# Optimization experiments

Measured on AMD Instinct MI355X. Metric: run time of the kernel, lower is better.

Reference implementation:

```python
import jax, jax.numpy as jnp
import numpy as np

N0, N1, N2, N3 = 8192, 32768, 65536, 65536
CUM = (N0, N0 + N1, N0 + N1 + N2, N0 + N1 + N2 + N3)  # nodes through hop k
NTOT = CUM[3]
EH = (131072, 262144, 262144)                          # edges per hop (per edge type)
ECUM = (EH[0], EH[0] + EH[1], EH[0] + EH[1] + EH[2])
ETOT = ECUM[2]
C, H, T = 64, 256, 3
HH = H // 2
B, L = 16, 512  # N0 == B * L: equal-length note sequences per graph
LN_EPS = 1e-5


def _ln(x, w, b):
    m = x.mean(-1, keepdims=True)
    v = x.var(-1, keepdims=True)
    return (x - m) / jnp.sqrt(v + LN_EPS) * w + b


def _seg_mean(msgs, dst, n):
    s = jax.ops.segment_sum(msgs, dst, num_segments=n)
    cnt = jax.ops.segment_sum(jnp.ones(dst.shape, msgs.dtype), dst, num_segments=n)
    return s / jnp.maximum(cnt, 1.0)[:, None]


def _l2(x):
    return x / jnp.maximum(jnp.linalg.norm(x, axis=-1, keepdims=True), 1e-12)


def _gru_dir(x, wih, whh, bih, bhh, reverse):
    # x: [B, Lt, Din]; torch gate order (r, z, n)
    gi = jnp.einsum('bld,gd->blg', x, wih) + bih
    gi = jnp.moveaxis(gi, 1, 0)  # [Lt, B, 3*HH]
    h0 = jnp.zeros((x.shape[0], HH), x.dtype)

    def step(h, g):
        gh = h @ whh.T + bhh
        ir, iz, in_ = jnp.split(g, 3, -1)
        hr, hz, hn = jnp.split(gh, 3, -1)
        r = jax.nn.sigmoid(ir + hr)
        z = jax.nn.sigmoid(iz + hz)
        n = jnp.tanh(in_ + r * hn)
        hnew = (1.0 - z) * n + z * h
        return hnew, hnew

    _, ys = jax.lax.scan(step, h0, gi, reverse=reverse)
    return jnp.moveaxis(ys, 0, 1)  # [B, Lt, HH]


def _bigru(x, wih, whh, bih, bhh):
    f = _gru_dir(x, wih[0], whh[0], bih[0], bhh[0], False)
    bwd = _gru_dir(x, wih[1], whh[1], bih[1], bhh[1], True)
    return jnp.concatenate([f, bwd], -1)


def _forward(x, edge_index, batch_size, sage0_proj_w, sage0_proj_b, sage0_lw, sage0_lb,
             sage0_rw, sage_lw, sage_lb, sage_rw, ln_w, ln_b,
             gru_wih0, gru_whh0, gru_bih0, gru_bhh0,
             gru_wih1, gru_whh1, gru_bih1, gru_bhh1,
             rnn_norm_w, rnn_norm_b, mlp1_w, mlp1_b, mlp_ln_w, mlp_ln_b,
             mlp2_w, mlp2_b, cat_w, cat_b):
    # ---- hybrid GRU branch on seed notes (equal lengths -> pad == reshape) ----
    xs = x[:batch_size].reshape(B, L, C)
    h = _bigru(xs, gru_wih0, gru_whh0, gru_bih0, gru_bhh0)
    h = _bigru(h, gru_wih1, gru_whh1, gru_bih1, gru_bhh1)  # inter-layer dropout: eval mode
    h = _ln(h, rnn_norm_w, rnn_norm_b)
    h = _ln(jax.nn.relu(h @ mlp1_w + mlp1_b), mlp_ln_w, mlp_ln_b) @ mlp2_w + mlp2_b
    x_rnn = h.reshape(batch_size, H)

    # ---- GNN layer 0: SAGEConv(project=True, normalize=True), hetero mean over T types ----
    feat = x
    outs = []
    for t in range(T):
        src, dst = edge_index[t, 0], edge_index[t, 1]
        xp = jax.nn.relu(feat @ sage0_proj_w[t] + sage0_proj_b[t])
        agg = _seg_mean(xp[src], dst, NTOT)
        outs.append(_l2(agg @ sage0_lw[t] + sage0_lb[t] + feat @ sage0_rw[t]))
    feat = sum(outs) / T
    feat = _ln(jax.nn.relu(feat), ln_w[0], ln_b[0])  # dropout: eval mode (identity)

    # ---- layers 1..2 with trim_to_layer: drop last sampled hop each layer ----
    n_layer = (CUM[2], CUM[1])
    e_layer = (ECUM[1], ECUM[0])
    for i in range(2):
        n, e = n_layer[i], e_layer[i]
        feat = feat[:n]
        outs = []
        for t in range(T):
            src, dst = edge_index[t, 0, :e], edge_index[t, 1, :e]
            agg = _seg_mean(feat[src], dst, n)
            outs.append(agg @ sage_lw[i, t] + sage_lb[i, t] + feat @ sage_rw[i, t])
        feat = sum(outs) / T
        if i == 0:
            feat = _ln(jax.nn.relu(feat), ln_w[1], ln_b[1])
    x_gnn = feat[:batch_size]
    return jnp.concatenate([x_rnn, x_gnn], -1) @ cat_w + cat_b


def setup_inputs():
    key = jax.random.key(0)
    ks = iter(jax.random.split(key, 64))

    def nrm(shape, fan_in):
        return jax.random.normal(next(ks), shape, jnp.float32) / float(np.sqrt(fan_in))

    # hop-structured edges: hop k has src < CUM[k+1], dst < CUM[k]
    ei = []
    for t in range(T):
        rows, cols = [], []
        for k in range(3):
            rows.append(jax.random.randint(next(ks), (EH[k],), 0, CUM[k + 1]))
            cols.append(jax.random.randint(next(ks), (EH[k],), 0, CUM[k]))
        ei.append(jnp.stack([jnp.concatenate(rows), jnp.concatenate(cols)]))
    edge_index = jnp.stack(ei).astype(jnp.int32)

    return dict(
        x=jax.random.normal(next(ks), (NTOT, C), jnp.float32),
        edge_index=edge_index,
        batch=(jnp.arange(N0) // L).astype(jnp.int32),
        batch_size=N0,
        sage0_proj_w=nrm((T, C, C), C), sage0_proj_b=jnp.zeros((T, C), jnp.float32),
        sage0_lw=nrm((T, C, H), C), sage0_lb=jnp.zeros((T, H), jnp.float32),
        sage0_rw=nrm((T, C, H), C),
        sage_lw=nrm((2, T, H, H), H), sage_lb=jnp.zeros((2, T, H), jnp.float32),
        sage_rw=nrm((2, T, H, H), H),
        ln_w=jnp.ones((2, H), jnp.float32), ln_b=jnp.zeros((2, H), jnp.float32),
        gru_wih0=nrm((2, 3 * HH, C), C), gru_whh0=nrm((2, 3 * HH, HH), HH),
        gru_bih0=jnp.zeros((2, 3 * HH), jnp.float32), gru_bhh0=jnp.zeros((2, 3 * HH), jnp.float32),
        gru_wih1=nrm((2, 3 * HH, H), H), gru_whh1=nrm((2, 3 * HH, HH), HH),
        gru_bih1=jnp.zeros((2, 3 * HH), jnp.float32), gru_bhh1=jnp.zeros((2, 3 * HH), jnp.float32),
        rnn_norm_w=jnp.ones((H,), jnp.float32), rnn_norm_b=jnp.zeros((H,), jnp.float32),
        mlp1_w=nrm((H, H), H), mlp1_b=jnp.zeros((H,), jnp.float32),
        mlp_ln_w=jnp.ones((H,), jnp.float32), mlp_ln_b=jnp.zeros((H,), jnp.float32),
        mlp2_w=nrm((H, H), H), mlp2_b=jnp.zeros((H,), jnp.float32),
        cat_w=nrm((2 * H, H), 2 * H), cat_b=jnp.zeros((H,), jnp.float32),
    )


def reference(x, edge_index, batch, batch_size, sage0_proj_w, sage0_proj_b, sage0_lw,
              sage0_lb, sage0_rw, sage_lw, sage_lb, sage_rw, ln_w, ln_b,
              gru_wih0, gru_whh0, gru_bih0, gru_bhh0, gru_wih1, gru_whh1, gru_bih1,
              gru_bhh1, rnn_norm_w, rnn_norm_b, mlp1_w, mlp1_b, mlp_ln_w, mlp_ln_b,
              mlp2_w, mlp2_b, cat_w, cat_b):
    # batch encodes 16 equal-length (512) sequences; bincount/pad == reshape above
    return _forward(x, edge_index, batch_size, sage0_proj_w, sage0_proj_b, sage0_lw,
                    sage0_lb, sage0_rw, sage_lw, sage_lb, sage_rw, ln_w, ln_b,
                    gru_wih0, gru_whh0, gru_bih0, gru_bhh0, gru_wih1, gru_whh1,
                    gru_bih1, gru_bhh1, rnn_norm_w, rnn_norm_b, mlp1_w, mlp1_b,
                    mlp_ln_w, mlp_ln_b, mlp2_w, mlp2_b, cat_w, cat_b)
```

## Files before the change

kernel.cpp:

```cpp
#include <hip/hip_runtime.h>
#include <stdint.h>

typedef unsigned short u16;
typedef __attribute__((ext_vector_type(8))) short short8;
typedef __attribute__((ext_vector_type(4))) short short4v;
typedef __attribute__((ext_vector_type(4))) float float4v;

#define DEV static __device__ __forceinline__

DEV float bf2f(u16 u){ union { unsigned int i; float f; } c; c.i = ((unsigned int)u) << 16; return c.f; }
DEV u16 f2bf(float f){ union { float ff; unsigned int i; } c; c.ff = f;
  unsigned int x = c.i; return (u16)((x + 0x7fffu + ((x >> 16) & 1u)) >> 16); }

#define MFMA16(a,b,c) __builtin_amdgcn_mfma_f32_16x16x32_bf16((a),(b),(c),0,0,0)

#define ETOTC  655360
#define TSTRIDE 155648
#define NBINS   466944

struct SM {
  u16 As[64*72];
  u16 Bs[256*72];
  float redS[4][64];
  float redQ[4][64];
  float rowA[64], rowB[64];
};

__global__ void detect_dtype(const u16* __restrict__ xs, int* __restrict__ flag){
  __shared__ int sh[256];
  int t = threadIdx.x; int cnt = 0;
  for (int i = t; i < 4096; i += 256){
    u16 u = xs[i]; int e = (u >> 7) & 0xff;
    cnt += (u == 0 || (e >= 112 && e <= 143)) ? 1 : 0;
  }
  sh[t] = cnt; __syncthreads();
  for (int d = 128; d; d >>= 1){ if (t < d) sh[t] += sh[t+d]; __syncthreads(); }
  if (t == 0) flag[0] = (sh[0] >= 3686) ? 1 : 0;
}

DEV u16 scrub(u16 v){ int e = (v >> 7) & 0xff; return (e == 0xff) ? (u16)0 : v; }

struct WSrc { const void* p[28]; };
__device__ const int g_wcum[29] = {0,12288,12480,61632,62400,111552,504768,506304,899520,
  900032,900544,949696,1048000,1048768,1049536,1246144,1344448,1345216,1345984,1346240,
  1346496,1412032,1412288,1412544,1412800,1478336,1478592,1609664,1609920};

__global__ void convert_all(const void* __restrict__ xin, WSrc d,
                            const int* __restrict__ flag, u16* __restrict__ xout,
                            u16* __restrict__ wout){
  int b = blockIdx.x;
  if (b < 10752){
    int i = b*256 + threadIdx.x;
    u16 v[4];
    if (flag[0] == 1){
      short4v s = ((const short4v*)xin)[i];
#pragma unroll
      for (int j=0;j<4;j++) v[j] = scrub((u16)s[j]);
    } else {
      float4v f = ((const float4v*)xin)[i];
#pragma unroll
      for (int j=0;j<4;j++) v[j] = scrub(f2bf(f[j]));
    }
    short4v o; o[0]=(short)v[0]; o[1]=(short)v[1]; o[2]=(short)v[2]; o[3]=(short)v[3];
    ((short4v*)xout)[i] = o;
  } else {
    int i = (b - 10752)*256 + threadIdx.x;
    if (i >= 1609920) return;
    int lo = 0, hi = 28;
    while (hi - lo > 1){ int m = (lo+hi) >> 1; if (i >= g_wcum[m]) lo = m; else hi = m; }
    int off = i - g_wcum[lo];
    u16 v = (flag[0] == 1) ? ((const u16*)d.p[lo])[off]
                           : f2bf(((const float*)d.p[lo])[off]);
    wout[i] = scrub(v);
  }
}

__global__ void packT(const u16* __restrict__ in, u16* __restrict__ out, int K, int N){
  int i = blockIdx.x*256 + threadIdx.x;
  if (i < K*N){ int n = i / K, k = i - n*K; out[i] = in[(size_t)k*N + n]; }
}

__global__ void pack_lr(const u16* __restrict__ lw, const u16* __restrict__ rw,
                        u16* __restrict__ out, int F){
  int K2 = 2*F; long total = 3L*256*K2;
  long i = (long)blockIdx.x*256 + threadIdx.x;
  if (i < total){
    int k = (int)(i % K2); int n = (int)((i / K2) & 255); int t = (int)(i / ((long)K2*256));
    out[i] = (k < F) ? lw[((size_t)t*F + k)*256 + n]
                     : rw[((size_t)t*F + (k-F))*256 + n];
  }
}

DEV void hist_body(int gb, const int* __restrict__ ei, int* __restrict__ cnt){
  int g = gb*256 + threadIdx.x;
  int t = g / ETOTC, e = g - t*ETOTC;
  int dst = ei[(size_t)t*2*ETOTC + ETOTC + e];
  int base = t*TSTRIDE;
  atomicAdd(&cnt[base + dst], 1);
  if (e < 393216) atomicAdd(&cnt[base + 106496 + dst], 1);
  if (e < 131072) atomicAdd(&cnt[base + 147456 + dst], 1);
}

DEV void perm_body(int gb, const int* __restrict__ ei, const int* __restrict__ off,
                   int* __restrict__ slot, int* __restrict__ srcs){
  int g = gb*256 + threadIdx.x;
  int t = g / ETOTC, e = g - t*ETOTC;
  int dst = ei[(size_t)t*2*ETOTC + ETOTC + e];
  int src = ei[(size_t)t*2*ETOTC + e];
  int base = t*TSTRIDE;
  { int b = base + dst; srcs[off[b] + atomicAdd(&slot[b], 1)] = src; }
  if (e < 393216){ int b = base + 106496 + dst;
    srcs[off[b] + atomicAdd(&slot[b], 1)] = src; }
  if (e < 131072){ int b = base + 147456 + dst;
    srcs[off[b] + atomicAdd(&slot[b], 1)] = src; }
}

__global__ void scan_blocks(const int* __restrict__ cnt, int* __restrict__ off,
                            int* __restrict__ bsum, int n){
  __shared__ int sh[256];
  int t = threadIdx.x;
  int base = blockIdx.x*2048 + t*8;
  int v[8]; int tot = 0;
#pragma unroll
  for (int j=0;j<8;j++){ v[j] = (base+j < n) ? cnt[base+j] : 0; tot += v[j]; }
  sh[t] = tot; __syncthreads();
  for (int d=1; d<256; d<<=1){
    int y = (t>=d) ? sh[t-d] : 0; __syncthreads();
    sh[t] += y; __syncthreads();
  }
  int run = sh[t] - tot;
#pragma unroll
  for (int j=0;j<8;j++){ if (base+j < n) off[base+j] = run; run += v[j]; }
  if (t == 255) bsum[blockIdx.x] = sh[255];
}

__global__ void scan_top(int* __restrict__ bsum, int G){
  __shared__ int sh[256];
  int t = threadIdx.x;
  int v = (t < G) ? bsum[t] : 0;
  sh[t] = v; __syncthreads();
  for (int d=1; d<256; d<<=1){
    int y = (t>=d) ? sh[t-d] : 0; __syncthreads();
    sh[t] += y; __syncthreads();
  }
  if (t < G) bsum[t] = sh[t] - v;
}

__global__ void scan_add(int* __restrict__ off, const int* __restrict__ bsum, int n){
  int add = bsum[blockIdx.x];
  int base = blockIdx.x*2048 + threadIdx.x*8;
#pragma unroll
  for (int j=0;j<8;j++) if (base+j < n) off[base+j] += add;
}

template<int F>
DEV void gather_body(int w, int lane,
    const int* __restrict__ off, const int* __restrict__ cnt, const int* __restrict__ srcs,
    const u16* __restrict__ feat, int ld, u16* __restrict__ out)
{
  int st = off[w], c = cnt[w];
  float sc = 1.f / (float)(c < 1 ? 1 : c);
  if (F == 64) {
    float a = 0.f, b = 0.f;
    int i = 0;
    for (; i + 4 <= c; i += 4){
      int s0 = srcs[st+i], s1 = srcs[st+i+1], s2 = srcs[st+i+2], s3 = srcs[st+i+3];
      u16 u0 = feat[(size_t)s0*ld + lane];
      u16 u1 = feat[(size_t)s1*ld + lane];
      u16 u2 = feat[(size_t)s2*ld + lane];
      u16 u3 = feat[(size_t)s3*ld + lane];
      a += bf2f(u0) + bf2f(u1);
      b += bf2f(u2) + bf2f(u3);
    }
    for (; i < c; ++i){ int s = srcs[st+i]; a += bf2f(feat[(size_t)s*ld + lane]); }
    out[(size_t)w*64 + lane] = f2bf((a + b)*sc);
  } else {
    float a0=0.f,a1=0.f,a2=0.f,a3=0.f;
    float b0=0.f,b1=0.f,b2=0.f,b3=0.f;
    int i = 0;
    for (; i + 4 <= c; i += 4){
      int s0 = srcs[st+i], s1 = srcs[st+i+1], s2 = srcs[st+i+2], s3 = srcs[st+i+3];
      short4v u0 = *(const short4v*)(feat + (size_t)s0*ld + lane*4);
      short4v u1 = *(const short4v*)(feat + (size_t)s1*ld + lane*4);
      short4v u2 = *(const short4v*)(feat + (size_t)s2*ld + lane*4);
      short4v u3 = *(const short4v*)(feat + (size_t)s3*ld + lane*4);
      a0 += bf2f((u16)u0[0]) + bf2f((u16)u1[0]);
      a1 += bf2f((u16)u0[1]) + bf2f((u16)u1[1]);
      a2 += bf2f((u16)u0[2]) + bf2f((u16)u1[2]);
      a3 += bf2f((u16)u0[3]) + bf2f((u16)u1[3]);
      b0 += bf2f((u16)u2[0]) + bf2f((u16)u3[0]);
      b1 += bf2f((u16)u2[1]) + bf2f((u16)u3[1]);
      b2 += bf2f((u16)u2[2]) + bf2f((u16)u3[2]);
      b3 += bf2f((u16)u2[3]) + bf2f((u16)u3[3]);
    }
    for (; i < c; ++i){
      int s = srcs[st+i];
      short4v u = *(const short4v*)(feat + (size_t)s*ld + lane*4);
      a0 += bf2f((u16)u[0]); a1 += bf2f((u16)u[1]);
      a2 += bf2f((u16)u[2]); a3 += bf2f((u16)u[3]);
    }
    u16* o = out + (size_t)w*256 + lane*4;
    o[0]=f2bf((a0+b0)*sc); o[1]=f2bf((a1+b1)*sc);
    o[2]=f2bf((a2+b2)*sc); o[3]=f2bf((a3+b3)*sc);
  }
}

DEV void ln_body(int r, int lane,
    const u16* __restrict__ in, u16* __restrict__ out,
    const u16* __restrict__ w, const u16* __restrict__ b)
{
  short4v u = *(const short4v*)(in + (size_t)r*256 + lane*4);
  float v[4];
#pragma unroll
  for (int i=0;i<4;i++) v[i] = bf2f((u16)u[i]);
  float s = v[0]+v[1]+v[2]+v[3];
  float q = v[0]*v[0]+v[1]*v[1]+v[2]*v[2]+v[3]*v[3];
#pragma unroll
  for (int d=1; d<64; d<<=1){ s += __shfl_xor(s, d); q += __shfl_xor(q, d); }
  float mu = s * (1.f/256.f);
  float var = fmaxf(q * (1.f/256.f) - mu*mu, 0.f);
  float rs = rsqrtf(var + 1e-5f);
  u16* o = out + (size_t)r*256 + lane*4;
#pragma unroll
  for (int i=0;i<4;i++){
    int col = lane*4 + i;
    o[i] = f2bf((v[i]-mu)*rs*bf2f(w[col]) + bf2f(b[col]));
  }
}

#define LGKM0_SB do{ asm volatile("s_waitcnt lgkmcnt(0)" ::: "memory"); \
                     __builtin_amdgcn_sched_barrier(0); \
                     __builtin_amdgcn_s_barrier(); \
                     __builtin_amdgcn_sched_barrier(0); }while(0)

#define GRU_STEP(S, C0, C1, C2) do{                                          \
    const int l_ = dir ? (511 - (S)) : (S);                                  \
    short8 afr_[4];                                                          \
    _Pragma("unroll")                                                        \
    for (int kt=0; kt<4; kt++) afr_[kt] = *(const short8*)(&hbf[kt*32 + lg*8]); \
    float4v acc_[4];                                                         \
    _Pragma("unroll")                                                        \
    for (int nt=0; nt<4; nt++) acc_[nt] = (float4v){0.f,0.f,0.f,0.f};        \
    _Pragma("unroll")                                                        \
    for (int kt=0; kt<4; kt++){                                              \
      _Pragma("unroll")                                                      \
      for (int nt=0; nt<4; nt++) acc_[nt] = MFMA16(afr_[kt], bfrag[nt][kt], acc_[nt]); } \
    if (lane < 16){                                                          \
      _Pragma("unroll")                                                      \
      for (int nt=0; nt<4; nt++) ghs[64*w + nt*16 + lane] = acc_[nt][0];     \
    }                                                                        \
    LGKM0_SB;                                                                \
    if (tid < 128){                                                          \
      float ghr = ghs[tid]       + bhr;                                      \
      float ghz = ghs[128 + tid] + bhz;                                      \
      float ghn = ghs[256 + tid] + bhn;                                      \
      float r_ = 1.f/(1.f + __expf(-((C0) + ghr)));                          \
      float z_ = 1.f/(1.f + __expf(-((C1) + ghz)));                          \
      float xn_ = (C2) + r_*ghn;                                             \
      float th_ = 1.f - 2.f/(__expf(2.f*xn_) + 1.f);                         \
      hreg = (1.f - z_)*th_ + z_*hreg;                                       \
      u16 hb_ = f2bf(hreg);                                                  \
      hbf[tid] = hb_;                                                        \
      hout[((size_t)(b*512 + l_))*256 + dir*128 + tid] = hb_;                \
      int sn_ = (S) + 2;                                                     \
      if (sn_ < 512){                                                        \
        int ln2_ = dir ? (511 - sn_) : sn_;                                  \
        const float* g_ = gbase + (size_t)ln2_*768;                          \
        (C0) = g_[0]; (C1) = g_[128]; (C2) = g_[256];                        \
      }                                                                      \
    }                                                                        \
    LGKM0_SB;                                                                \
  }while(0)

DEV void gru_body(const float* __restrict__ gi, const u16* __restrict__ whh,
                  const u16* __restrict__ bhh, u16* __restrict__ hout,
                  int bid, u16* hbf, float* ghs)
{
  const int b = bid >> 1, dir = bid & 1;
  const int tid = threadIdx.x;
  const int w = tid >> 6, lane = tid & 63;
  const int lr = lane & 15, lg = lane >> 4;

  short8 bfrag[4][4];
#pragma unroll
  for (int nt=0; nt<4; nt++)
#pragma unroll
    for (int kt=0; kt<4; kt++){
      int n = 64*w + nt*16 + lr;
      bfrag[nt][kt] = *(const short8*)(whh + ((size_t)(dir*384 + n))*128 + kt*32 + lg*8);
    }

  const float* gbase = gi + (size_t)b*512*768 + dir*384 + tid;
  float hreg = 0.f, bhr = 0.f, bhz = 0.f, bhn = 0.f;
  float a0=0.f,a1=0.f,a2=0.f, e0=0.f,e1=0.f,e2=0.f;
  if (tid < 128){
    bhr = bf2f(bhh[dir*384 + tid]);
    bhz = bf2f(bhh[dir*384 + 128 + tid]);
    bhn = bf2f(bhh[dir*384 + 256 + tid]);
    const float* g0 = gbase + (size_t)(dir ? 511 : 0)*768;
    a0 = g0[0]; a1 = g0[128]; a2 = g0[256];
    const float* g1 = gbase + (size_t)(dir ? 510 : 1)*768;
    e0 = g1[0]; e1 = g1[128]; e2 = g1[256];
  }
  if (tid < 64) ((unsigned int*)hbf)[tid] = 0u;
  LGKM0_SB;

  for (int s2 = 0; s2 < 512; s2 += 2){
    GRU_STEP(s2,     a0, a1, a2);
    GRU_STEP(s2 + 1, e0, e1, e2);
  }
}

template<int F>
__global__ __launch_bounds__(384,1) void fused_gru_gather(
    const float* __restrict__ gi, const u16* __restrict__ whh,
    const u16* __restrict__ bhh, u16* __restrict__ hout,
    const int* __restrict__ off0, const int* __restrict__ cnt0, const int* __restrict__ srcs,
    const u16* __restrict__ feat, int ld, int featstep,
    u16* __restrict__ aggout, long aggstride, int rows, int bpt)
{
  __shared__ u16 hbf[128];
  __shared__ float ghs[384];
  if (blockIdx.x < 32){
    gru_body(gi, whh, bhh, hout, blockIdx.x, hbf, ghs);
    return;
  }
  int gb = blockIdx.x - 32;
  int t = gb / bpt, rb = gb - t*bpt;
  int w = rb*6 + (threadIdx.x >> 6);
  int lane = threadIdx.x & 63;
  if (w >= rows) return;
  gather_body<F>(w, lane, off0 + t*TSTRIDE, cnt0 + t*TSTRIDE, srcs,
                 feat + (size_t)t*featstep, ld, aggout + (size_t)t*aggstride);
}

template<int EPI, bool OUTF32>
DEV void gemm_body(SM& sm, int bx, int by,
    const u16* __restrict__ A, int lda,
    const u16* __restrict__ WT, int K, int N,
    const u16* __restrict__ bias,
    const u16* __restrict__ lnw, const u16* __restrict__ lnb,
    void* __restrict__ Cp, int ldc, const int* __restrict__ dynof)
{
  u16* As = sm.As; u16* Bs = sm.Bs;
  const int tid = threadIdx.x;
  const int lane = tid & 63, wid = tid >> 6;
  const int lr = lane & 15, lg = lane >> 4;
  const int m0 = bx * 64;
  const int col0 = by * 256;
  float4v acc[4][4];
#pragma unroll
  for (int i=0;i<4;i++)
#pragma unroll
    for (int j=0;j<4;j++) acc[i][j] = (float4v){0.f,0.f,0.f,0.f};

  for (int k0 = 0; k0 < K; k0 += 64){
#pragma unroll
    for (int v = 0; v < 2; v++){
      int idx = tid + v*256; int r = idx >> 3, c8 = (idx & 7) << 3;
      *(short8*)(&As[r*72 + c8]) = *(const short8*)(A + (size_t)(m0+r)*lda + k0 + c8);
    }
#pragma unroll
    for (int v = 0; v < 8; v++){
      int idx = tid + v*256; int nn = idx >> 3, c8 = (idx & 7) << 3;
      short8 val = {0,0,0,0,0,0,0,0};
      if (col0 + nn < N) val = *(const short8*)(WT + (size_t)(col0+nn)*K + k0 + c8);
      *(short8*)(&Bs[nn*72 + c8]) = val;
    }
    __syncthreads();
#pragma unroll
    for (int kk = 0; kk < 2; kk++){
      short8 af[4], bfr[4];
#pragma unroll
      for (int i=0;i<4;i++) af[i]  = *(const short8*)(&As[(16*i+lr)*72 + kk*32 + lg*8]);
#pragma unroll
      for (int j=0;j<4;j++) bfr[j] = *(const short8*)(&Bs[(wid*64+16*j+lr)*72 + kk*32 + lg*8]);
#pragma unroll
      for (int i=0;i<4;i++)
#pragma unroll
        for (int j=0;j<4;j++) acc[i][j] = MFMA16(af[i], bfr[j], acc[i][j]);
    }
    __syncthreads();
  }
  int cols[4];
#pragma unroll
  for (int j=0;j<4;j++) cols[j] = col0 + wid*64 + 16*j + lr;
#pragma unroll
  for (int j=0;j<4;j++){
    float bv = (cols[j] < N) ? bf2f(bias[cols[j]]) : 0.f;
#pragma unroll
    for (int i=0;i<4;i++)
#pragma unroll
      for (int r=0;r<4;r++) acc[i][j][r] += bv;
  }
  if (EPI >= 1){
#pragma unroll
    for (int i=0;i<4;i++)
#pragma unroll
      for (int j=0;j<4;j++)
#pragma unroll
        for (int r=0;r<4;r++) acc[i][j][r] = fmaxf(acc[i][j][r], 0.f);
  }
  if (EPI == 2){
#pragma unroll
    for (int i=0;i<4;i++)
#pragma unroll
      for (int r=0;r<4;r++){
        float p = acc[i][0][r]+acc[i][1][r]+acc[i][2][r]+acc[i][3][r];
        float q = acc[i][0][r]*acc[i][0][r]+acc[i][1][r]*acc[i][1][r]
                 +acc[i][2][r]*acc[i][2][r]+acc[i][3][r]*acc[i][3][r];
#pragma unroll
        for (int d=1; d<16; d<<=1){ p += __shfl_xor(p,d); q += __shfl_xor(q,d); }
        if (lr == 0){ sm.redS[wid][16*i + lg*4 + r] = p; sm.redQ[wid][16*i + lg*4 + r] = q; }
      }
    __syncthreads();
    if (tid < 64){
      float s = sm.redS[0][tid]+sm.redS[1][tid]+sm.redS[2][tid]+sm.redS[3][tid];
      float q = sm.redQ[0][tid]+sm.redQ[1][tid]+sm.redQ[2][tid]+sm.redQ[3][tid];
      float mu = s * (1.f/256.f);
      float var = fmaxf(q * (1.f/256.f) - mu*mu, 0.f);
      sm.rowA[tid] = mu; sm.rowB[tid] = rsqrtf(var + 1e-5f);
    }
    __syncthreads();
#pragma unroll
    for (int i=0;i<4;i++)
#pragma unroll
      for (int r=0;r<4;r++){
        int rl = 16*i + lg*4 + r;
        float mu = sm.rowA[rl], rs = sm.rowB[rl];
#pragma unroll
        for (int j=0;j<4;j++){
          float w = bf2f(lnw[cols[j]]), bb = bf2f(lnb[cols[j]]);
          acc[i][j][r] = (acc[i][j][r]-mu)*rs*w + bb;
        }
      }
  }
  bool of32 = OUTF32;
  if (dynof) of32 = (dynof[0] == 0);
#pragma unroll
  for (int i=0;i<4;i++)
#pragma unroll
    for (int r=0;r<4;r++){
      int row = m0 + 16*i + lg*4 + r;
#pragma unroll
      for (int j=0;j<4;j++) if (cols[j] < N){
        if (of32) ((float*)Cp)[(size_t)row*ldc + cols[j]] = acc[i][j][r];
        else ((u16*)Cp)[(size_t)row*ldc + cols[j]] = f2bf(acc[i][j][r]);
      }
    }
}

template<int EPI, bool OUTF32>
__global__ __launch_bounds__(256,1) void gemm_bt(
    const u16* __restrict__ A, int lda,
    const u16* __restrict__ WT, int K, int N,
    const u16* __restrict__ bias,
    const u16* __restrict__ lnw, const u16* __restrict__ lnb,
    void* __restrict__ Cp, int ldc, const int* __restrict__ dynof)
{
  __shared__ SM sm;
  gemm_body<EPI,OUTF32>(sm, blockIdx.x, blockIdx.y, A, lda, WT, K, N, bias, lnw, lnb, Cp, ldc, dynof);
}

template<int F, bool DO_L2, bool DO_LN>
DEV void sage_body(SM& sm, int bx,
    const u16* __restrict__ A1, long a1t, const u16* __restrict__ A2, int lda2,
    const u16* __restrict__ WTp, const u16* __restrict__ lbp,
    const u16* __restrict__ lnw, const u16* __restrict__ lnb,
    u16* __restrict__ out, int ldc, int outcol)
{
  constexpr int K2 = 2*F;
  u16* As = sm.As; u16* Bs = sm.Bs;
  const int tid = threadIdx.x;
  const int lane = tid & 63, wid = tid >> 6;
  const int lr = lane & 15, lg = lane >> 4;
  const int m0 = bx * 64;
  int colsL[4];
#pragma unroll
  for (int j=0;j<4;j++) colsL[j] = wid*64 + 16*j + lr;
  float4v facc[4][4];
#pragma unroll
  for (int i=0;i<4;i++)
#pragma unroll
    for (int j=0;j<4;j++) facc[i][j] = (float4v){0.f,0.f,0.f,0.f};

  for (int t=0; t<3; ++t){
    float4v acc[4][4];
#pragma unroll
    for (int i=0;i<4;i++)
#pragma unroll
      for (int j=0;j<4;j++) acc[i][j] = (float4v){0.f,0.f,0.f,0.f};
    const u16* WT  = WTp + (size_t)t*256*K2;
    const u16* A1b = A1 + (size_t)t*a1t;
    for (int k0 = 0; k0 < K2; k0 += 64){
      const u16* Ab; int la, kb;
      if (k0 < F){ Ab = A1b; la = F; kb = k0; } else { Ab = A2; la = lda2; kb = k0 - F; }
#pragma unroll
      for (int v=0; v<2; v++){
        int idx = tid + v*256; int r = idx >> 3, c8 = (idx & 7) << 3;
        *(short8*)(&As[r*72 + c8]) = *(const short8*)(Ab + (size_t)(m0+r)*la + kb + c8);
      }
#pragma unroll
      for (int v=0; v<8; v++){
        int idx = tid + v*256; int nn = idx >> 3, c8 = (idx & 7) << 3;
        *(short8*)(&Bs[nn*72 + c8]) = *(const short8*)(WT + (size_t)nn*K2 + k0 + c8);
      }
      __syncthreads();
#pragma unroll
      for (int kk = 0; kk < 2; kk++){
        short8 af[4], bfr[4];
#pragma unroll
        for (int i=0;i<4;i++) af[i]  = *(const short8*)(&As[(16*i+lr)*72 + kk*32 + lg*8]);
#pragma unroll
        for (int j=0;j<4;j++) bfr[j] = *(const short8*)(&Bs[(wid*64+16*j+lr)*72 + kk*32 + lg*8]);
#pragma unroll
        for (int i=0;i<4;i++)
#pragma unroll
          for (int j=0;j<4;j++) acc[i][j] = MFMA16(af[i], bfr[j], acc[i][j]);
      }
      __syncthreads();
    }
#pragma unroll
    for (int j=0;j<4;j++){
      float bv = bf2f(lbp[t*256 + colsL[j]]);
#pragma unroll
      for (int i=0;i<4;i++)
#pragma unroll
        for (int r=0;r<4;r++) acc[i][j][r] += bv;
    }
    if (DO_L2){
#pragma unroll
      for (int i=0;i<4;i++)
#pragma unroll
        for (int r=0;r<4;r++){
          float q = acc[i][0][r]*acc[i][0][r]+acc[i][1][r]*acc[i][1][r]
                   +acc[i][2][r]*acc[i][2][r]+acc[i][3][r]*acc[i][3][r];
#pragma unroll
          for (int d=1; d<16; d<<=1) q += __shfl_xor(q,d);
          if (lr == 0) sm.redQ[wid][16*i + lg*4 + r] = q;
        }
      __syncthreads();
      if (tid < 64){
        float q = sm.redQ[0][tid]+sm.redQ[1][tid]+sm.redQ[2][tid]+sm.redQ[3][tid];
        sm.rowA[tid] = 1.f / fmaxf(sqrtf(q), 1e-12f);
      }
      __syncthreads();
#pragma unroll
      for (int i=0;i<4;i++)
#pragma unroll
        for (int r=0;r<4;r++){
          float sc = sm.rowA[16*i + lg*4 + r];
#pragma unroll
          for (int j=0;j<4;j++) acc[i][j][r] *= sc;
        }
      __syncthreads();
    }
#pragma unroll
    for (int i=0;i<4;i++)
#pragma unroll
      for (int j=0;j<4;j++)
#pragma unroll
        for (int r=0;r<4;r++) facc[i][j][r] += acc[i][j][r];
  }
  const float inv3 = (1.f/3.f);
#pragma unroll
  for (int i=0;i<4;i++)
#pragma unroll
    for (int j=0;j<4;j++)
#pragma unroll
      for (int r=0;r<4;r++) facc[i][j][r] *= inv3;
  if (DO_LN){
#pragma unroll
    for (int i=0;i<4;i++)
#pragma unroll
      for (int j=0;j<4;j++)
#pragma unroll
        for (int r=0;r<4;r++) facc[i][j][r] = fmaxf(facc[i][j][r], 0.f);
#pragma unroll
    for (int i=0;i<4;i++)
#pragma unroll
      for (int r=0;r<4;r++){
        float p = facc[i][0][r]+facc[i][1][r]+facc[i][2][r]+facc[i][3][r];
        float q = facc[i][0][r]*facc[i][0][r]+facc[i][1][r]*facc[i][1][r]
                 +facc[i][2][r]*facc[i][2][r]+facc[i][3][r]*facc[i][3][r];
#pragma unroll
        for (int d=1; d<16; d<<=1){ p += __shfl_xor(p,d); q += __shfl_xor(q,d); }
        if (lr == 0){ sm.redS[wid][16*i + lg*4 + r] = p; sm.redQ[wid][16*i + lg*4 + r] = q; }
      }
    __syncthreads();
    if (tid < 64){
      float s = sm.redS[0][tid]+sm.redS[1][tid]+sm.redS[2][tid]+sm.redS[3][tid];
      float q = sm.redQ[0][tid]+sm.redQ[1][tid]+sm.redQ[2][tid]+sm.redQ[3][tid];
      float mu = s * (1.f/256.f);
      float var = fmaxf(q * (1.f/256.f) - mu*mu, 0.f);
      sm.rowA[tid] = mu; sm.rowB[tid] = rsqrtf(var + 1e-5f);
    }
    __syncthreads();
#pragma unroll
    for (int i=0;i<4;i++)
#pragma unroll
      for (int r=0;r<4;r++){
        int rl = 16*i + lg*4 + r;
        float mu = sm.rowA[rl], rs = sm.rowB[rl];
#pragma unroll
        for (int j=0;j<4;j++){
          float w = bf2f(lnw[colsL[j]]), bb = bf2f(lnb[colsL[j]]);
          facc[i][j][r] = (facc[i][j][r]-mu)*rs*w + bb;
        }
      }
  }
#pragma unroll
  for (int i=0;i<4;i++)
#pragma unroll
    for (int r=0;r<4;r++){
      int row = m0 + 16*i + lg*4 + r;
#pragma unroll
      for (int j=0;j<4;j++)
        out[(size_t)row*ldc + outcol + colsL[j]] = f2bf(facc[i][j][r]);
    }
}

__global__ __launch_bounds__(256,1) void fused_wih0_hist(
    const u16* __restrict__ x16, const u16* __restrict__ wih0b, const u16* __restrict__ bih0b,
    float* __restrict__ GI, const int* __restrict__ ei, int* __restrict__ CNT)
{
  __shared__ SM sm;
  int b = blockIdx.x;
  if (b < 384)
    gemm_body<0,true>(sm, b & 127, b >> 7, x16, 64, wih0b, 64, 768, bih0b,
                      nullptr, nullptr, GI, 768, nullptr);
  else
    hist_body(b - 384, ei, CNT);
}

__global__ __launch_bounds__(256,1) void fused_xp_perm(
    const u16* __restrict__ x16, const u16* __restrict__ WXP, const u16* __restrict__ projb,
    u16* __restrict__ XP3,
    const int* __restrict__ ei, const int* __restrict__ OFF,
    int* __restrict__ SLOT, int* __restrict__ SRCS)
{
  __shared__ SM sm;
  int b = blockIdx.x;
  if (b < 2688)
    gemm_body<1,false>(sm, b, 0, x16, 64, WXP, 64, 192, projb,
                       nullptr, nullptr, XP3, 192, nullptr);
  else
    perm_body(b - 2688, ei, OFF, SLOT, SRCS);
}

__global__ __launch_bounds__(256,1) void fused_gemm_sage0(
    const u16* __restrict__ H0, const u16* __restrict__ wih1b, const u16* __restrict__ bih1b,
    float* __restrict__ GI,
    const u16* __restrict__ AGGB0, const u16* __restrict__ x16, const u16* __restrict__ WP0,
    const u16* __restrict__ s0lb, const u16* __restrict__ lnw, const u16* __restrict__ lnb,
    u16* __restrict__ FEAT)
{
  __shared__ SM sm;
  int b = blockIdx.x;
  if (b < 384)
    gemm_body<0,true>(sm, b & 127, b >> 7, H0, 256, wih1b, 256, 768, bih1b,
                      nullptr, nullptr, GI, 768, nullptr);
  else
    sage_body<64,true,true>(sm, b - 384, AGGB0, (long)106496*64, x16, 64, WP0, s0lb,
                            lnw, lnb, FEAT, 256, 0);
}

__global__ __launch_bounds__(256,1) void fused_ln_sage1(
    const u16* __restrict__ AGGB1, const u16* __restrict__ FEAT, const u16* __restrict__ WP1,
    const u16* __restrict__ slb, const u16* __restrict__ lnw, const u16* __restrict__ lnb,
    u16* __restrict__ FEAT2,
    const u16* __restrict__ H1, u16* __restrict__ HA,
    const u16* __restrict__ rnw, const u16* __restrict__ rnb)
{
  __shared__ SM sm;
  int b = blockIdx.x;
  if (b < 640)
    sage_body<256,false,true>(sm, b, AGGB1, (long)40960*256, FEAT, 256, WP1, slb,
                              lnw, lnb, FEAT2, 256, 0);
  else {
    int r = (b - 640)*4 + (threadIdx.x >> 6);
    ln_body(r, threadIdx.x & 63, H1, HA, rnw, rnb);
  }
}

__global__ __launch_bounds__(256,1) void fused_mlp1_gather2(
    const u16* __restrict__ HA, const u16* __restrict__ M1T, const u16* __restrict__ mlp1b,
    const u16* __restrict__ mlnw, const u16* __restrict__ mlnb, u16* __restrict__ HB,
    const int* __restrict__ OFF, const int* __restrict__ CNT, const int* __restrict__ SRCS,
    const u16* __restrict__ FEAT2, u16* __restrict__ AGGB2)
{
  __shared__ SM sm;
  int b = blockIdx.x;
  if (b < 128){
    gemm_body<2,false>(sm, b, 0, HA, 256, M1T, 256, 256, mlp1b, mlnw, mlnb, HB, 256, nullptr);
  } else {
    int g = b - 128;
    int t = g / 2048, rb = g - t*2048;
    int w = rb*4 + (threadIdx.x >> 6);
    int lane = threadIdx.x & 63;
    if (w < 8192)
      gather_body<256>(w, lane, OFF + t*TSTRIDE + 147456, CNT + t*TSTRIDE + 147456, SRCS,
                       FEAT2, 256, AGGB2 + (size_t)t*8192*256);
  }
}

__global__ __launch_bounds__(256,1) void fused_mlp2_sage2(
    const u16* __restrict__ HB, const u16* __restrict__ M2T, const u16* __restrict__ mlp2b,
    u16* __restrict__ CAT,
    const u16* __restrict__ AGGB2, const u16* __restrict__ FEAT2, const u16* __restrict__ WP2,
    const u16* __restrict__ slb2)
{
  __shared__ SM sm;
  int b = blockIdx.x;
  if (b < 128)
    gemm_body<0,false>(sm, b, 0, HB, 256, M2T, 256, 256, mlp2b, nullptr, nullptr, CAT, 512, nullptr);
  else
    sage_body<256,false,false>(sm, b - 128, AGGB2, (long)8192*256, FEAT2, 256, WP2, slb2,
                               nullptr, nullptr, CAT, 512, 256);
}

extern "C" void kernel_launch(void* const* d_in, const int* in_sizes, int n_in,
                              void* d_out, int out_size, void* d_ws, size_t ws_size,
                              hipStream_t stream)
{
  (void)in_sizes; (void)n_in; (void)out_size;
  const int* ei = (const int*)d_in[1];

  char* ws = (char*)d_ws;
  size_t o = 0;
  auto alloc = [&](size_t b){ size_t p = o; o += (b + 255) & ~(size_t)255; return p; };
  char* RA   = ws + alloc(66060288);
  u16* XP3   = (u16*)RA;
  u16* AGGB1 = (u16*)RA;
  char* RR   = ws + alloc(41943040);
  float* GI  = (float*)RR;
  u16* H0    = (u16*)(RR + 25165824);
  u16* H1    = (u16*)(RR + 29360128);
  u16* HA    = (u16*)(RR + 33554432);
  u16* HB    = (u16*)(RR + 37748736);
  char* RB   = ws + alloc(40894464);
  u16* AGGB0 = (u16*)RB;
  u16* AGGB2 = (u16*)RB;
  u16* FEAT2 = (u16*)(RB + 12582912);
  u16* FEAT  = (u16*)(ws + alloc(106496ull*256*2));
  u16* CAT   = (u16*)(ws + alloc(8192ull*512*2));
  u16* AR    = (u16*)(ws + alloc(12619968ull*2));
  u16* WXP   = (u16*)(ws + alloc(192ull*64*2));
  u16* WP0   = (u16*)(ws + alloc(3ull*256*128*2));
  u16* WP1   = (u16*)(ws + alloc(3ull*256*512*2));
  u16* WP2   = (u16*)(ws + alloc(3ull*256*512*2));
  u16* M1T   = (u16*)(ws + alloc(256ull*256*2));
  u16* M2T   = (u16*)(ws + alloc(256ull*256*2));
  u16* CTT   = (u16*)(ws + alloc(256ull*512*2));
  int* CNT   = (int*)(ws + alloc((size_t)NBINS*4));
  int* OFF   = (int*)(ws + alloc((size_t)NBINS*4));
  int* SLOT  = (int*)(ws + alloc((size_t)NBINS*4));
  int* BSUM  = (int*)(ws + alloc(256ull*4));
  int* SRCS  = (int*)(ws + alloc(3538944ull*4));
  int* FLAG  = (int*)(ws + alloc(256));
  if (o > ws_size) return;

  u16* x16    = AR;
  u16* projw6 = AR + 11010048; u16* projb6 = AR + 11022336;
  u16* s0lw6  = AR + 11022528; u16* s0lb6  = AR + 11071680; u16* s0rw6 = AR + 11072448;
  u16* slw6   = AR + 11121600; u16* slb6   = AR + 11514816; u16* srw6  = AR + 11516352;
  u16* lnw6   = AR + 11909568; u16* lnb6   = AR + 11910080;
  u16* wih0b  = AR + 11910592; u16* whh0b  = AR + 11959744;
  u16* bih0b  = AR + 12058048; u16* bhh0b  = AR + 12058816;
  u16* wih1b  = AR + 12059584; u16* whh1b  = AR + 12256192;
  u16* bih1b  = AR + 12354496; u16* bhh1b  = AR + 12355264;
  u16* rnw6   = AR + 12356032; u16* rnb6   = AR + 12356288;
  u16* mlp1w6 = AR + 12356544; u16* mlp1b6 = AR + 12422080;
  u16* mlnw6  = AR + 12422336; u16* mlnb6  = AR + 12422592;
  u16* mlp2w6 = AR + 12422848; u16* mlp2b6 = AR + 12488384;
  u16* catw6  = AR + 12488640; u16* catb6  = AR + 12619712;

  detect_dtype<<<dim3(1),dim3(256),0,stream>>>((const u16*)d_in[0], FLAG);
  WSrc wsrc;
  for (int i=0;i<28;i++) wsrc.p[i] = d_in[4+i];
  convert_all<<<dim3(10752 + 6289),dim3(256),0,stream>>>(d_in[0], wsrc, FLAG, x16, AR + 11010048);

  hipMemsetAsync(CNT, 0, (size_t)NBINS*4, stream);
  hipMemsetAsync(SLOT, 0, (size_t)NBINS*4, stream);
  packT<<<dim3(256),dim3(256),0,stream>>>(mlp1w6, M1T, 256, 256);
  packT<<<dim3(256),dim3(256),0,stream>>>(mlp2w6, M2T, 256, 256);
  packT<<<dim3(512),dim3(256),0,stream>>>(catw6,  CTT, 512, 256);
  for (int t=0;t<3;t++)
    packT<<<dim3(16),dim3(256),0,stream>>>(projw6 + (size_t)t*4096, WXP + (size_t)t*4096, 64, 64);
  pack_lr<<<dim3(384),dim3(256),0,stream>>>(s0lw6, s0rw6, WP0, 64);
  pack_lr<<<dim3(1536),dim3(256),0,stream>>>(slw6,               srw6,               WP1, 256);
  pack_lr<<<dim3(1536),dim3(256),0,stream>>>(slw6 + 3ull*256*256, srw6 + 3ull*256*256, WP2, 256);

  fused_wih0_hist<<<dim3(384 + 7680),dim3(256),0,stream>>>(
      x16, wih0b, bih0b, GI, ei, CNT);

  scan_blocks<<<dim3(228),dim3(256),0,stream>>>(CNT, OFF, BSUM, NBINS);
  scan_top<<<dim3(1),dim3(256),0,stream>>>(BSUM, 228);
  scan_add<<<dim3(228),dim3(256),0,stream>>>(OFF, BSUM, NBINS);

  fused_xp_perm<<<dim3(2688 + 7680),dim3(256),0,stream>>>(
      x16, WXP, projb6, XP3, ei, OFF, SLOT, SRCS);

  fused_gru_gather<64><<<dim3(32 + 3*17750),dim3(384),0,stream>>>(
      GI, whh0b, bhh0b, H0,
      OFF, CNT, SRCS, XP3, 192, 64, AGGB0, (long)106496*64, 106496, 17750);

  fused_gemm_sage0<<<dim3(2048),dim3(256),0,stream>>>(
      H0, wih1b, bih1b, GI,
      AGGB0, x16, WP0, s0lb6, lnw6, lnb6, FEAT);

  fused_gru_gather<256><<<dim3(32 + 3*6827),dim3(384),0,stream>>>(
      GI, whh1b, bhh1b, H1,
      OFF + 106496, CNT + 106496, SRCS, FEAT, 256, 0, AGGB1, (long)40960*256, 40960, 6827);

  fused_ln_sage1<<<dim3(2688),dim3(256),0,stream>>>(
      AGGB1, FEAT, WP1, slb6, lnw6+256, lnb6+256, FEAT2,
      H1, HA, rnw6, rnb6);

  fused_mlp1_gather2<<<dim3(6272),dim3(256),0,stream>>>(
      HA, M1T, mlp1b6, mlnw6, mlnb6, HB,
      OFF, CNT, SRCS, FEAT2, AGGB2);

  fused_mlp2_sage2<<<dim3(256),dim3(256),0,stream>>>(
      HB, M2T, mlp2b6, CAT,
      AGGB2, FEAT2, WP2, slb6 + 3*256);

  gemm_bt<0,false><<<dim3(128,1),dim3(256),0,stream>>>(CAT, 512, CTT, 512, 256, catb6,
      nullptr, nullptr, d_out, 256, FLAG);
}
```

Before: 1.536 ms.

## Process two GRU sequences per block sharing recurrent weight fragments

Each GRU block now advances two batch sequences of the same direction at once, reusing the register-resident Whh fragments for two MFMA chains and using 256 threads for the gate update. This halves the number of GRU blocks (16 instead of 32), freeing CUs for the overlapped gather work and doubling MFMA work per serial step without adding barriers. The risk is a longer per-step latency per block, since twice the MFMAs plus wider shared memory traffic sit on the sequential critical path.

```diff
diff --git a/kernel.cpp b/kernel.cpp
--- a/kernel.cpp
+++ b/kernel.cpp
@@ -233,39 +233,47 @@
                      __builtin_amdgcn_s_barrier(); \
                      __builtin_amdgcn_sched_barrier(0); }while(0)
 
-#define GRU_STEP(S, C0, C1, C2) do{                                          \
+#define GRU_STEPD(S, C0, C1, C2) do{                                         \
     const int l_ = dir ? (511 - (S)) : (S);                                  \
-    short8 afr_[4];                                                          \
+    float4v accA_[4], accB_[4];                                              \
     _Pragma("unroll")                                                        \
-    for (int kt=0; kt<4; kt++) afr_[kt] = *(const short8*)(&hbf[kt*32 + lg*8]); \
-    float4v acc_[4];                                                         \
-    _Pragma("unroll")                                                        \
-    for (int nt=0; nt<4; nt++) acc_[nt] = (float4v){0.f,0.f,0.f,0.f};        \
+    for (int nt=0; nt<4; nt++){ accA_[nt] = (float4v){0.f,0.f,0.f,0.f};      \
+                                accB_[nt] = (float4v){0.f,0.f,0.f,0.f}; }    \
     _Pragma("unroll")                                                        \
     for (int kt=0; kt<4; kt++){                                              \
+      short8 aA_ = *(const short8*)(&hbf[kt*32 + lg*8]);                     \
+      short8 aB_ = *(const short8*)(&hbf[128 + kt*32 + lg*8]);               \
       _Pragma("unroll")                                                      \
-      for (int nt=0; nt<4; nt++) acc_[nt] = MFMA16(afr_[kt], bfrag[nt][kt], acc_[nt]); } \
+      for (int nt=0; nt<4; nt++){                                            \
+        accA_[nt] = MFMA16(aA_, bfrag[nt][kt], accA_[nt]);                   \
+        accB_[nt] = MFMA16(aB_, bfrag[nt][kt], accB_[nt]);                   \
+      }                                                                      \
+    }                                                                        \
     if (lane < 16){                                                          \
       _Pragma("unroll")                                                      \
-      for (int nt=0; nt<4; nt++) ghs[64*w + nt*16 + lane] = acc_[nt][0];     \
+      for (int nt=0; nt<4; nt++){                                            \
+        ghs[64*w + nt*16 + lane]       = accA_[nt][0];                       \
+        ghs[384 + 64*w + nt*16 + lane] = accB_[nt][0];                       \
+      }                                                                      \
     }                                                                        \
     LGKM0_SB;                                                                \
-    if (tid < 128){                                                          \
-      float ghr = ghs[tid]       + bhr;                                      \
-      float ghz = ghs[128 + tid] + bhz;                                      \
-      float ghn = ghs[256 + tid] + bhn;                                      \
+    if (tid < 256){                                                          \
+      const float* gp_ = ghs + cid*384;                                      \
+      float ghr = gp_[hidx]       + bhr;                                     \
+      float ghz = gp_[128 + hidx] + bhz;                                     \
+      float ghn = gp_[256 + hidx] + bhn;                                     \
       float r_ = 1.f/(1.f + __expf(-((C0) + ghr)));                          \
       float z_ = 1.f/(1.f + __expf(-((C1) + ghz)));                          \
       float xn_ = (C2) + r_*ghn;                                             \
       float th_ = 1.f - 2.f/(__expf(2.f*xn_) + 1.f);                         \
       hreg = (1.f - z_)*th_ + z_*hreg;                                       \
       u16 hb_ = f2bf(hreg);                                                  \
-      hbf[tid] = hb_;                                                        \
-      hout[((size_t)(b*512 + l_))*256 + dir*128 + tid] = hb_;                \
+      hbf[cid*128 + hidx] = hb_;                                             \
+      hout[((size_t)(bb*512 + l_))*256 + dir*128 + hidx] = hb_;              \
       int sn_ = (S) + 2;                                                     \
       if (sn_ < 512){                                                        \
         int ln2_ = dir ? (511 - sn_) : sn_;                                  \
-        const float* g_ = gbase + (size_t)ln2_*768;                          \
+        const float* g_ = gbase + (size_t)ln2_*768;                         \
         (C0) = g_[0]; (C1) = g_[128]; (C2) = g_[256];                        \
       }                                                                      \
     }                                                                        \
@@ -274,12 +282,15 @@
 
 DEV void gru_body(const float* __restrict__ gi, const u16* __restrict__ whh,
                   const u16* __restrict__ bhh, u16* __restrict__ hout,
-                  int bid, u16* hbf, float* ghs)
-{
-  const int b = bid >> 1, dir = bid & 1;
+                  int bid, u16* hbf , float* ghs )
+{
+  const int q = bid >> 1, dir = bid & 1;
   const int tid = threadIdx.x;
   const int w = tid >> 6, lane = tid & 63;
   const int lr = lane & 15, lg = lane >> 4;
+  const int cid = (tid >> 7) & 1;
+  const int hidx = tid & 127;
+  const int bb = 2*q + cid;
 
   short8 bfrag[4][4];
 #pragma unroll
@@ -290,24 +301,24 @@
       bfrag[nt][kt] = *(const short8*)(whh + ((size_t)(dir*384 + n))*128 + kt*32 + lg*8);
     }
 
-  const float* gbase = gi + (size_t)b*512*768 + dir*384 + tid;
+  const float* gbase = gi + (size_t)bb*512*768 + dir*384 + hidx;
   float hreg = 0.f, bhr = 0.f, bhz = 0.f, bhn = 0.f;
   float a0=0.f,a1=0.f,a2=0.f, e0=0.f,e1=0.f,e2=0.f;
-  if (tid < 128){
-    bhr = bf2f(bhh[dir*384 + tid]);
-    bhz = bf2f(bhh[dir*384 + 128 + tid]);
-    bhn = bf2f(bhh[dir*384 + 256 + tid]);
+  if (tid < 256){
+    bhr = bf2f(bhh[dir*384 + hidx]);
+    bhz = bf2f(bhh[dir*384 + 128 + hidx]);
+    bhn = bf2f(bhh[dir*384 + 256 + hidx]);
     const float* g0 = gbase + (size_t)(dir ? 511 : 0)*768;
     a0 = g0[0]; a1 = g0[128]; a2 = g0[256];
     const float* g1 = gbase + (size_t)(dir ? 510 : 1)*768;
     e0 = g1[0]; e1 = g1[128]; e2 = g1[256];
   }
-  if (tid < 64) ((unsigned int*)hbf)[tid] = 0u;
+  if (tid < 128) ((unsigned int*)hbf)[tid] = 0u;
   LGKM0_SB;
 
   for (int s2 = 0; s2 < 512; s2 += 2){
-    GRU_STEP(s2,     a0, a1, a2);
-    GRU_STEP(s2 + 1, e0, e1, e2);
+    GRU_STEPD(s2,     a0, a1, a2);
+    GRU_STEPD(s2 + 1, e0, e1, e2);
   }
 }
 
@@ -319,13 +330,13 @@
     const u16* __restrict__ feat, int ld, int featstep,
     u16* __restrict__ aggout, long aggstride, int rows, int bpt)
 {
-  __shared__ u16 hbf[128];
-  __shared__ float ghs[384];
-  if (blockIdx.x < 32){
+  __shared__ u16 hbf[256];
+  __shared__ float ghs[768];
+  if (blockIdx.x < 16){
     gru_body(gi, whh, bhh, hout, blockIdx.x, hbf, ghs);
     return;
   }
-  int gb = blockIdx.x - 32;
+  int gb = blockIdx.x - 16;
   int t = gb / bpt, rb = gb - t*bpt;
   int w = rb*6 + (threadIdx.x >> 6);
   int lane = threadIdx.x & 63;
@@ -801,7 +812,7 @@
   fused_xp_perm<<<dim3(2688 + 7680),dim3(256),0,stream>>>(
       x16, WXP, projb6, XP3, ei, OFF, SLOT, SRCS);
 
-  fused_gru_gather<64><<<dim3(32 + 3*17750),dim3(384),0,stream>>>(
+  fused_gru_gather<64><<<dim3(16 + 3*17750),dim3(384),0,stream>>>(
       GI, whh0b, bhh0b, H0,
       OFF, CNT, SRCS, XP3, 192, 64, AGGB0, (long)106496*64, 106496, 17750);
 
@@ -809,7 +820,7 @@
       H0, wih1b, bih1b, GI,
       AGGB0, x16, WP0, s0lb6, lnw6, lnb6, FEAT);
 
-  fused_gru_gather<256><<<dim3(32 + 3*6827),dim3(384),0,stream>>>(
+  fused_gru_gather<256><<<dim3(16 + 3*6827),dim3(384),0,stream>>>(
       GI, whh1b, bhh1b, H1,
       OFF + 106496, CNT + 106496, SRCS, FEAT, 256, 0, AGGB1, (long)40960*256, 40960, 6827);
 
```

Result: slower. 1.819 ms (+18.4%).
